# Performance work log

Measured on AMD Instinct MI355X. Metric: run time of the kernel, lower is better.

## Reference

```python
import jax, jax.numpy as jnp
import numpy as np

B, S, H, E, TOPK = 16384, 64, 256, 8, 2


def setup_inputs() -> dict:
    key = jax.random.key(0)
    k1, k2, k3, k4 = jax.random.split(key, 4)
    x = jax.random.normal(k1, (B, S, H), dtype=jnp.float32)
    xr = jax.random.normal(k2, (B, H), dtype=jnp.float32)
    W_router = jax.random.normal(k3, (H, E), dtype=jnp.float32) * 0.02
    W_experts = jax.random.normal(k4, (E, H, H), dtype=jnp.float32) * 0.02
    b_experts = jnp.zeros((E, H), dtype=jnp.float32)
    return {"x": x, "xr": xr, "W_router": W_router,
            "W_experts": W_experts, "b_experts": b_experts}


def reference(x, xr, W_router, W_experts, b_experts):
    # Routing network: logits [B, E]
    logits = xr @ W_router
    # top-2 expert selection; softmax over the two selected logits (as in torch code)
    top_vals, top_idx = jax.lax.top_k(logits, TOPK)          # [B, 2]
    w = jax.nn.softmax(top_vals, axis=1)                     # [B, 2]
    # Dense gate matrix [B, E]: scatter top-2 weights into expert slots
    gate = jnp.zeros_like(logits).at[jnp.arange(x.shape[0])[:, None], top_idx].add(w)
    # Expert forward: pooled token representation -> per-expert dense tanh
    pooled = x.mean(axis=1)                                  # [B, H]
    h_all = jnp.tanh(jnp.einsum('bh,ehd->bed', pooled, W_experts) + b_experts[None])
    # Weighted scatter-add combine: prediction[b] += w * hidden_states
    prediction = jnp.einsum('be,beh->bh', gate, h_all)       # [B, H]
    return prediction
```

## Files before the change

kernel.cpp:

```cpp
#include <hip/hip_runtime.h>
#include <hip/hip_bf16.h>

constexpr int Bn = 16384;
constexpr int S  = 64;
constexpr int H  = 256;
constexpr int E  = 8;

constexpr int RPB  = 32;
constexpr int CBLK = Bn / RPB;
constexpr int TPB  = 512;
constexpr int PSTR = H + 8;

typedef short bf16x8 __attribute__((ext_vector_type(8)));
typedef float f32x4  __attribute__((ext_vector_type(4)));

__device__ __forceinline__ float fast_tanh(float x) {
    const float ex = __expf(2.0f * x);
    return (ex - 1.0f) / (ex + 1.0f);
}

__global__ __launch_bounds__(256) void prep_wfrag(const float* __restrict__ We,
                                                  __hip_bfloat16* __restrict__ Wf) {
    __shared__ __hip_bfloat16 tile[64][H + 4];
    const int e    = blockIdx.x >> 2;
    const int hblk = blockIdx.x & 3;
    const int t    = threadIdx.x;

    const float* src = We + ((size_t)e * H + hblk * 64) * H;
#pragma unroll
    for (int i = 0; i < 16; ++i) {
        const int idx = t + 256 * i;
        const int hh  = idx >> 6;
        const int c4  = idx & 63;
        float4 v = reinterpret_cast<const float4*>(src + (size_t)hh * H)[c4];
        tile[hh][c4 * 4 + 0] = __float2bfloat16(v.x);
        tile[hh][c4 * 4 + 1] = __float2bfloat16(v.y);
        tile[hh][c4 * 4 + 2] = __float2bfloat16(v.z);
        tile[hh][c4 * 4 + 3] = __float2bfloat16(v.w);
    }
    __syncthreads();

#pragma unroll
    for (int i = 0; i < 8; ++i) {
        const int task = i * 256 + t;
        const int kk2  = task >> 10;
        const int nt   = (task >> 6) & 15;
        const int l    = task & 63;
        const int kk   = hblk * 2 + kk2;
        const int hlb  = kk2 * 32 + (l >> 4) * 8;
        const int d    = nt * 16 + (l & 15);
        bf16x8 p;
#pragma unroll
        for (int j = 0; j < 8; ++j) {
            __hip_bfloat16 hv = tile[hlb + j][d];
            p[j] = *reinterpret_cast<short*>(&hv);
        }
        reinterpret_cast<bf16x8*>(Wf)[(((size_t)(e * 8 + kk) * 16 + nt) * 64 + l)] = p;
    }
}

__global__ __launch_bounds__(256) void pool_kernel(const float* __restrict__ x,
                                                   __hip_bfloat16* __restrict__ pws) {
    const int t   = threadIdx.x;
    const int row = blockIdx.x * 4 + (t >> 6);
    const int c4  = t & 63;

    const float4* xrow = reinterpret_cast<const float4*>(x + (size_t)row * (S * H));
    float4 a0 = make_float4(0.f,0.f,0.f,0.f), a1 = a0, a2 = a0, a3 = a0;
#pragma unroll 16
    for (int s = 0; s < S; s += 4) {
        float4 v0 = xrow[(s + 0) * 64 + c4];
        float4 v1 = xrow[(s + 1) * 64 + c4];
        float4 v2 = xrow[(s + 2) * 64 + c4];
        float4 v3 = xrow[(s + 3) * 64 + c4];
        a0.x += v0.x; a0.y += v0.y; a0.z += v0.z; a0.w += v0.w;
        a1.x += v1.x; a1.y += v1.y; a1.z += v1.z; a1.w += v1.w;
        a2.x += v2.x; a2.y += v2.y; a2.z += v2.z; a2.w += v2.w;
        a3.x += v3.x; a3.y += v3.y; a3.z += v3.z; a3.w += v3.w;
    }
    const float sc = 1.0f / (float)S;
    float r0 = (a0.x + a1.x) + (a2.x + a3.x);
    float r1 = (a0.y + a1.y) + (a2.y + a3.y);
    float r2 = (a0.z + a1.z) + (a2.z + a3.z);
    float r3 = (a0.w + a1.w) + (a2.w + a3.w);
    ushort4 pk;
    {
        __hip_bfloat16 h0 = __float2bfloat16(r0 * sc);
        __hip_bfloat16 h1 = __float2bfloat16(r1 * sc);
        __hip_bfloat16 h2 = __float2bfloat16(r2 * sc);
        __hip_bfloat16 h3 = __float2bfloat16(r3 * sc);
        pk.x = *reinterpret_cast<unsigned short*>(&h0);
        pk.y = *reinterpret_cast<unsigned short*>(&h1);
        pk.z = *reinterpret_cast<unsigned short*>(&h2);
        pk.w = *reinterpret_cast<unsigned short*>(&h3);
    }
    *reinterpret_cast<ushort4*>(pws + (size_t)row * H + c4 * 4) = pk;
}

__global__ __launch_bounds__(TPB, 4) void combine_kernel(
    const __hip_bfloat16* __restrict__ pws,
    const float* __restrict__ xr,
    const float* __restrict__ Wr,
    const float* __restrict__ be,
    const __hip_bfloat16* __restrict__ Wf,
    float* __restrict__ out)
{
    const int b0 = blockIdx.x * RPB;
    const int t  = threadIdx.x;

    __shared__ __hip_bfloat16 pooled[RPB][PSTR];
    __shared__ float logit_s[RPB][E];
    __shared__ float gate_s[RPB][E];

    {
        const __hip_bfloat16* src = pws + (size_t)b0 * H + t * 16;
#pragma unroll
        for (int u = 0; u < 2; ++u) {
            const int g = t * 16 + u * 8;
            bf16x8 v = *reinterpret_cast<const bf16x8*>(src + u * 8);
            *reinterpret_cast<bf16x8*>(&pooled[g >> 8][g & 255]) = v;
        }
    }

    if (t < RPB * E) {
        const int r = t >> 3, e = t & 7;
        const float* xrp = xr + (size_t)(b0 + r) * H;
        double acc = 0.0;
#pragma unroll 8
        for (int h = 0; h < H; ++h)
            acc += (double)xrp[h] * (double)Wr[h * E + e];
        logit_s[r][e] = (float)acc;
    }
    __syncthreads();

    if (t < RPB) {
        int i0 = 0; float v0 = logit_s[t][0];
#pragma unroll
        for (int e = 1; e < E; ++e)
            if (logit_s[t][e] > v0) { v0 = logit_s[t][e]; i0 = e; }
        int i1 = -1; float v1 = -3.0e38f;
#pragma unroll
        for (int e = 0; e < E; ++e) {
            if (e == i0) continue;
            if (logit_s[t][e] > v1) { v1 = logit_s[t][e]; i1 = e; }
        }
        const float ex  = expf(v1 - v0);
        const float inv = 1.0f / (1.0f + ex);
#pragma unroll
        for (int e = 0; e < E; ++e) gate_s[t][e] = 0.f;
        gate_s[t][i0] = inv;
        gate_s[t][i1] = ex * inv;
    }
    __syncthreads();

    {
        const int w  = t >> 6;
        const int l  = t & 63;
        const int rg = w >> 2;
        const int dg = w & 3;
        const int lr = l & 15;
        const int lq = l >> 4;

        f32x4 oacc[4];
#pragma unroll
        for (int n = 0; n < 4; ++n) oacc[n] = 0.f;

        const __hip_bfloat16* abase = &pooled[rg * 16 + lr][lq * 8];
        const bf16x8* wf8 = reinterpret_cast<const bf16x8*>(Wf);

        for (int e = 0; e < E; ++e) {
            f32x4 acc[4];
#pragma unroll
            for (int n = 0; n < 4; ++n) acc[n] = 0.f;

#pragma unroll
            for (int kk = 0; kk < 8; ++kk) {
                const bf16x8 a = *reinterpret_cast<const bf16x8*>(abase + kk * 32);
                const size_t kb = ((size_t)(e * 8 + kk) * 16 + dg * 4) * 64 + l;
                bf16x8 bfr[4];
#pragma unroll
                for (int n = 0; n < 4; ++n)
                    bfr[n] = wf8[kb + (size_t)n * 64];
#pragma unroll
                for (int n = 0; n < 4; ++n)
                    acc[n] = __builtin_amdgcn_mfma_f32_16x16x32_bf16(a, bfr[n], acc[n], 0, 0, 0);
            }

            float g[4];
#pragma unroll
            for (int j = 0; j < 4; ++j) g[j] = gate_s[rg * 16 + lq * 4 + j][e];
#pragma unroll
            for (int n = 0; n < 4; ++n) {
                const int d = dg * 64 + n * 16 + lr;
                const float bias = be[e * H + d];
#pragma unroll
                for (int j = 0; j < 4; ++j)
                    oacc[n][j] += g[j] * fast_tanh(acc[n][j] + bias);
            }
        }

#pragma unroll
        for (int n = 0; n < 4; ++n) {
            const int d = dg * 64 + n * 16 + lr;
#pragma unroll
            for (int j = 0; j < 4; ++j) {
                const int r = rg * 16 + lq * 4 + j;
                out[(size_t)(b0 + r) * H + d] = oacc[n][j];
            }
        }
    }
}

__global__ __launch_bounds__(256) void moe_fused_fallback(
    const float* __restrict__ x, const float* __restrict__ xr,
    const float* __restrict__ Wr, const float* __restrict__ We,
    const float* __restrict__ be, float* __restrict__ out)
{
    const int b = blockIdx.x;
    const int t = threadIdx.x;

    __shared__ float  pooled[H];
    __shared__ float  xr_s[H];
    __shared__ float4 red4[4][64];
    __shared__ float  logits_s[E];
    __shared__ int    sel[2];
    __shared__ float  wsel[2];

    {
        const float4* xrow = reinterpret_cast<const float4*>(x + (size_t)b * S * H);
        const int c4 = t & 63;
        const int sg = t >> 6;
        float4 acc = make_float4(0.f, 0.f, 0.f, 0.f);
#pragma unroll
        for (int i = 0; i < 16; ++i) {
            float4 v = xrow[(sg + 4 * i) * 64 + c4];
            acc.x += v.x; acc.y += v.y; acc.z += v.z; acc.w += v.w;
        }
        red4[sg][c4] = acc;
        xr_s[t] = xr[(size_t)b * H + t];
    }
    __syncthreads();
    {
        const float* r0 = reinterpret_cast<const float*>(&red4[0][0]);
        const float* r1 = reinterpret_cast<const float*>(&red4[1][0]);
        const float* r2 = reinterpret_cast<const float*>(&red4[2][0]);
        const float* r3 = reinterpret_cast<const float*>(&red4[3][0]);
        pooled[t] = (r0[t] + r1[t] + r2[t] + r3[t]) * (1.0f / (float)S);
    }
    if (t < E) {
        double acc = 0.0;
        for (int h = 0; h < H; ++h)
            acc += (double)xr_s[h] * (double)Wr[h * E + t];
        logits_s[t] = (float)acc;
    }
    __syncthreads();
    if (t == 0) {
        int i0 = 0; float v0 = logits_s[0];
        for (int e = 1; e < E; ++e)
            if (logits_s[e] > v0) { v0 = logits_s[e]; i0 = e; }
        int i1 = -1; float v1 = -3.0e38f;
        for (int e = 0; e < E; ++e) {
            if (e == i0) continue;
            if (logits_s[e] > v1) { v1 = logits_s[e]; i1 = e; }
        }
        const float ex = expf(v1 - v0);
        const float inv = 1.0f / (1.0f + ex);
        sel[0] = i0; sel[1] = i1;
        wsel[0] = inv; wsel[1] = ex * inv;
    }
    __syncthreads();
    {
        const int   e0 = sel[0], e1 = sel[1];
        const float w0 = wsel[0], w1 = wsel[1];
        const float* W0 = We + (size_t)e0 * H * H + t;
        const float* W1 = We + (size_t)e1 * H * H + t;
        float a0 = be[e0 * H + t];
        float a1 = be[e1 * H + t];
#pragma unroll 8
        for (int h = 0; h < H; ++h) {
            const float p = pooled[h];
            a0 = fmaf(p, W0[(size_t)h * H], a0);
            a1 = fmaf(p, W1[(size_t)h * H], a1);
        }
        out[(size_t)b * H + t] = w0 * tanhf(a0) + w1 * tanhf(a1);
    }
}

extern "C" void kernel_launch(void* const* d_in, const int* in_sizes, int n_in,
                              void* d_out, int out_size, void* d_ws, size_t ws_size,
                              hipStream_t stream) {
    const float* x  = (const float*)d_in[0];
    const float* xr = (const float*)d_in[1];
    const float* Wr = (const float*)d_in[2];
    const float* We = (const float*)d_in[3];
    const float* be = (const float*)d_in[4];
    float* out = (float*)d_out;

    (void)in_sizes; (void)n_in; (void)out_size;

    const size_t wf_elems = (size_t)E * H * H;
    const size_t need = (wf_elems + (size_t)Bn * H) * sizeof(__hip_bfloat16);
    if (ws_size >= need) {
        __hip_bfloat16* Wf  = (__hip_bfloat16*)d_ws;
        __hip_bfloat16* pws = Wf + wf_elems;
        prep_wfrag<<<32, 256, 0, stream>>>(We, Wf);
        pool_kernel<<<Bn / 4, 256, 0, stream>>>(x, pws);
        combine_kernel<<<CBLK, TPB, 0, stream>>>(pws, xr, Wr, be, Wf, out);
    } else {
        moe_fused_fallback<<<Bn, 256, 0, stream>>>(x, xr, Wr, We, be, out);
    }
}
```

Before: 275.7 us.

## Merge pool and weight-prep kernels; restructure combine to 4 waves with 2 row tiles

```diff
diff --git a/kernel.cpp b/kernel.cpp
--- a/kernel.cpp
+++ b/kernel.cpp
@@ -8,8 +8,10 @@
 
 constexpr int RPB  = 32;
 constexpr int CBLK = Bn / RPB;
-constexpr int TPB  = 512;
 constexpr int PSTR = H + 8;
+
+constexpr int POOLB = Bn / 4;
+constexpr int PREPB = E * 8;
 
 typedef short bf16x8 __attribute__((ext_vector_type(8)));
 typedef float f32x4  __attribute__((ext_vector_type(4)));
@@ -19,85 +21,81 @@
     return (ex - 1.0f) / (ex + 1.0f);
 }
 
-__global__ __launch_bounds__(256) void prep_wfrag(const float* __restrict__ We,
-                                                  __hip_bfloat16* __restrict__ Wf) {
-    __shared__ __hip_bfloat16 tile[64][H + 4];
-    const int e    = blockIdx.x >> 2;
-    const int hblk = blockIdx.x & 3;
-    const int t    = threadIdx.x;
-
-    const float* src = We + ((size_t)e * H + hblk * 64) * H;
-#pragma unroll
-    for (int i = 0; i < 16; ++i) {
-        const int idx = t + 256 * i;
-        const int hh  = idx >> 6;
-        const int c4  = idx & 63;
-        float4 v = reinterpret_cast<const float4*>(src + (size_t)hh * H)[c4];
-        tile[hh][c4 * 4 + 0] = __float2bfloat16(v.x);
-        tile[hh][c4 * 4 + 1] = __float2bfloat16(v.y);
-        tile[hh][c4 * 4 + 2] = __float2bfloat16(v.z);
-        tile[hh][c4 * 4 + 3] = __float2bfloat16(v.w);
-    }
-    __syncthreads();
-
-#pragma unroll
-    for (int i = 0; i < 8; ++i) {
-        const int task = i * 256 + t;
-        const int kk2  = task >> 10;
-        const int nt   = (task >> 6) & 15;
-        const int l    = task & 63;
-        const int kk   = hblk * 2 + kk2;
-        const int hlb  = kk2 * 32 + (l >> 4) * 8;
-        const int d    = nt * 16 + (l & 15);
-        bf16x8 p;
-#pragma unroll
-        for (int j = 0; j < 8; ++j) {
-            __hip_bfloat16 hv = tile[hlb + j][d];
-            p[j] = *reinterpret_cast<short*>(&hv);
-        }
-        reinterpret_cast<bf16x8*>(Wf)[(((size_t)(e * 8 + kk) * 16 + nt) * 64 + l)] = p;
-    }
-}
-
-__global__ __launch_bounds__(256) void pool_kernel(const float* __restrict__ x,
-                                                   __hip_bfloat16* __restrict__ pws) {
-    const int t   = threadIdx.x;
-    const int row = blockIdx.x * 4 + (t >> 6);
-    const int c4  = t & 63;
-
-    const float4* xrow = reinterpret_cast<const float4*>(x + (size_t)row * (S * H));
-    float4 a0 = make_float4(0.f,0.f,0.f,0.f), a1 = a0, a2 = a0, a3 = a0;
+__global__ __launch_bounds__(256) void stage1_kernel(
+    const float* __restrict__ x,
+    const float* __restrict__ We,
+    __hip_bfloat16* __restrict__ pws,
+    __hip_bfloat16* __restrict__ Wf)
+{
+    __shared__ __hip_bfloat16 tile[32][H + 4];
+    const int t = threadIdx.x;
+
+    if (blockIdx.x < POOLB) {
+        const int row = blockIdx.x * 4 + (t >> 6);
+        const int c4  = t & 63;
+
+        const f32x4* xrow = reinterpret_cast<const f32x4*>(x + (size_t)row * (S * H));
+        f32x4 a0 = 0.f, a1 = 0.f, a2 = 0.f, a3 = 0.f;
 #pragma unroll 16
-    for (int s = 0; s < S; s += 4) {
-        float4 v0 = xrow[(s + 0) * 64 + c4];
-        float4 v1 = xrow[(s + 1) * 64 + c4];
-        float4 v2 = xrow[(s + 2) * 64 + c4];
-        float4 v3 = xrow[(s + 3) * 64 + c4];
-        a0.x += v0.x; a0.y += v0.y; a0.z += v0.z; a0.w += v0.w;
-        a1.x += v1.x; a1.y += v1.y; a1.z += v1.z; a1.w += v1.w;
-        a2.x += v2.x; a2.y += v2.y; a2.z += v2.z; a2.w += v2.w;
-        a3.x += v3.x; a3.y += v3.y; a3.z += v3.z; a3.w += v3.w;
-    }
-    const float sc = 1.0f / (float)S;
-    float r0 = (a0.x + a1.x) + (a2.x + a3.x);
-    float r1 = (a0.y + a1.y) + (a2.y + a3.y);
-    float r2 = (a0.z + a1.z) + (a2.z + a3.z);
-    float r3 = (a0.w + a1.w) + (a2.w + a3.w);
-    ushort4 pk;
-    {
-        __hip_bfloat16 h0 = __float2bfloat16(r0 * sc);
-        __hip_bfloat16 h1 = __float2bfloat16(r1 * sc);
-        __hip_bfloat16 h2 = __float2bfloat16(r2 * sc);
-        __hip_bfloat16 h3 = __float2bfloat16(r3 * sc);
-        pk.x = *reinterpret_cast<unsigned short*>(&h0);
-        pk.y = *reinterpret_cast<unsigned short*>(&h1);
-        pk.z = *reinterpret_cast<unsigned short*>(&h2);
-        pk.w = *reinterpret_cast<unsigned short*>(&h3);
-    }
-    *reinterpret_cast<ushort4*>(pws + (size_t)row * H + c4 * 4) = pk;
-}
-
-__global__ __launch_bounds__(TPB, 4) void combine_kernel(
+        for (int s = 0; s < S; s += 4) {
+            f32x4 v0 = __builtin_nontemporal_load(xrow + (s + 0) * 64 + c4);
+            f32x4 v1 = __builtin_nontemporal_load(xrow + (s + 1) * 64 + c4);
+            f32x4 v2 = __builtin_nontemporal_load(xrow + (s + 2) * 64 + c4);
+            f32x4 v3 = __builtin_nontemporal_load(xrow + (s + 3) * 64 + c4);
+            a0 += v0; a1 += v1; a2 += v2; a3 += v3;
+        }
+        const f32x4 res = (a0 + a1) + (a2 + a3);
+        const float sc = 1.0f / (float)S;
+        ushort4 pk;
+        {
+            __hip_bfloat16 h0 = __float2bfloat16(res[0] * sc);
+            __hip_bfloat16 h1 = __float2bfloat16(res[1] * sc);
+            __hip_bfloat16 h2 = __float2bfloat16(res[2] * sc);
+            __hip_bfloat16 h3 = __float2bfloat16(res[3] * sc);
+            pk.x = *reinterpret_cast<unsigned short*>(&h0);
+            pk.y = *reinterpret_cast<unsigned short*>(&h1);
+            pk.z = *reinterpret_cast<unsigned short*>(&h2);
+            pk.w = *reinterpret_cast<unsigned short*>(&h3);
+        }
+        *reinterpret_cast<ushort4*>(pws + (size_t)row * H + c4 * 4) = pk;
+    } else {
+        const int bid = blockIdx.x - POOLB;
+        const int e   = bid >> 3;
+        const int kk  = bid & 7;
+
+        const float* src = We + ((size_t)e * H + kk * 32) * H;
+#pragma unroll
+        for (int i = 0; i < 8; ++i) {
+            const int idx = t + 256 * i;
+            const int hh  = idx >> 6;
+            const int c4  = idx & 63;
+            float4 v = reinterpret_cast<const float4*>(src + (size_t)hh * H)[c4];
+            tile[hh][c4 * 4 + 0] = __float2bfloat16(v.x);
+            tile[hh][c4 * 4 + 1] = __float2bfloat16(v.y);
+            tile[hh][c4 * 4 + 2] = __float2bfloat16(v.z);
+            tile[hh][c4 * 4 + 3] = __float2bfloat16(v.w);
+        }
+        __syncthreads();
+
+#pragma unroll
+        for (int i = 0; i < 4; ++i) {
+            const int task = i * 256 + t;
+            const int nt_  = task >> 6;
+            const int l    = task & 63;
+            const int hlb  = (l >> 4) * 8;
+            const int d    = nt_ * 16 + (l & 15);
+            bf16x8 p;
+#pragma unroll
+            for (int j = 0; j < 8; ++j) {
+                __hip_bfloat16 hv = tile[hlb + j][d];
+                p[j] = *reinterpret_cast<short*>(&hv);
+            }
+            reinterpret_cast<bf16x8*>(Wf)[(((size_t)(e * 8 + kk) * 16 + nt_) * 64 + l)] = p;
+        }
+    }
+}
+
+__global__ __launch_bounds__(256, 2) void combine_kernel(
     const __hip_bfloat16* __restrict__ pws,
     const float* __restrict__ xr,
     const float* __restrict__ Wr,
@@ -113,16 +111,16 @@
     __shared__ float gate_s[RPB][E];
 
     {
-        const __hip_bfloat16* src = pws + (size_t)b0 * H + t * 16;
-#pragma unroll
-        for (int u = 0; u < 2; ++u) {
-            const int g = t * 16 + u * 8;
+        const __hip_bfloat16* src = pws + (size_t)b0 * H + t * 32;
+#pragma unroll
+        for (int u = 0; u < 4; ++u) {
+            const int g = t * 32 + u * 8;
             bf16x8 v = *reinterpret_cast<const bf16x8*>(src + u * 8);
             *reinterpret_cast<bf16x8*>(&pooled[g >> 8][g & 255]) = v;
         }
     }
 
-    if (t < RPB * E) {
+    {
         const int r = t >> 3, e = t & 7;
         const float* xrp = xr + (size_t)(b0 + r) * H;
         double acc = 0.0;
@@ -154,60 +152,73 @@
     __syncthreads();
 
     {
-        const int w  = t >> 6;
+        const int dg = t >> 6;
         const int l  = t & 63;
-        const int rg = w >> 2;
-        const int dg = w & 3;
         const int lr = l & 15;
         const int lq = l >> 4;
 
-        f32x4 oacc[4];
-#pragma unroll
-        for (int n = 0; n < 4; ++n) oacc[n] = 0.f;
-
-        const __hip_bfloat16* abase = &pooled[rg * 16 + lr][lq * 8];
+        f32x4 oacc[2][4];
+#pragma unroll
+        for (int m = 0; m < 2; ++m)
+#pragma unroll
+            for (int n = 0; n < 4; ++n) oacc[m][n] = 0.f;
+
+        const __hip_bfloat16* a0base = &pooled[lr][lq * 8];
+        const __hip_bfloat16* a1base = &pooled[16 + lr][lq * 8];
         const bf16x8* wf8 = reinterpret_cast<const bf16x8*>(Wf);
 
         for (int e = 0; e < E; ++e) {
-            f32x4 acc[4];
-#pragma unroll
-            for (int n = 0; n < 4; ++n) acc[n] = 0.f;
+            f32x4 acc[2][4];
+#pragma unroll
+            for (int m = 0; m < 2; ++m)
+#pragma unroll
+                for (int n = 0; n < 4; ++n) acc[m][n] = 0.f;
 
 #pragma unroll
             for (int kk = 0; kk < 8; ++kk) {
-                const bf16x8 a = *reinterpret_cast<const bf16x8*>(abase + kk * 32);
+                const bf16x8 a0 = *reinterpret_cast<const bf16x8*>(a0base + kk * 32);
+                const bf16x8 a1 = *reinterpret_cast<const bf16x8*>(a1base + kk * 32);
                 const size_t kb = ((size_t)(e * 8 + kk) * 16 + dg * 4) * 64 + l;
                 bf16x8 bfr[4];
 #pragma unroll
                 for (int n = 0; n < 4; ++n)
                     bfr[n] = wf8[kb + (size_t)n * 64];
 #pragma unroll
-                for (int n = 0; n < 4; ++n)
-                    acc[n] = __builtin_amdgcn_mfma_f32_16x16x32_bf16(a, bfr[n], acc[n], 0, 0, 0);
+                for (int n = 0; n < 4; ++n) {
+                    acc[0][n] = __builtin_amdgcn_mfma_f32_16x16x32_bf16(a0, bfr[n], acc[0][n], 0, 0, 0);
+                    acc[1][n] = __builtin_amdgcn_mfma_f32_16x16x32_bf16(a1, bfr[n], acc[1][n], 0, 0, 0);
+                }
             }
 
-            float g[4];
-#pragma unroll
-            for (int j = 0; j < 4; ++j) g[j] = gate_s[rg * 16 + lq * 4 + j][e];
+            float g[2][4];
+#pragma unroll
+            for (int m = 0; m < 2; ++m)
+#pragma unroll
+                for (int j = 0; j < 4; ++j)
+                    g[m][j] = gate_s[m * 16 + lq * 4 + j][e];
 #pragma unroll
             for (int n = 0; n < 4; ++n) {
                 const int d = dg * 64 + n * 16 + lr;
                 const float bias = be[e * H + d];
 #pragma unroll
-                for (int j = 0; j < 4; ++j)
-                    oacc[n][j] += g[j] * fast_tanh(acc[n][j] + bias);
+                for (int m = 0; m < 2; ++m)
+#pragma unroll
+                    for (int j = 0; j < 4; ++j)
+                        oacc[m][n][j] += g[m][j] * fast_tanh(acc[m][n][j] + bias);
             }
         }
 
 #pragma unroll
-        for (int n = 0; n < 4; ++n) {
-            const int d = dg * 64 + n * 16 + lr;
-#pragma unroll
-            for (int j = 0; j < 4; ++j) {
-                const int r = rg * 16 + lq * 4 + j;
-                out[(size_t)(b0 + r) * H + d] = oacc[n][j];
+        for (int m = 0; m < 2; ++m)
+#pragma unroll
+            for (int n = 0; n < 4; ++n) {
+                const int d = dg * 64 + n * 16 + lr;
+#pragma unroll
+                for (int j = 0; j < 4; ++j) {
+                    const int r = m * 16 + lq * 4 + j;
+                    out[(size_t)(b0 + r) * H + d] = oacc[m][n][j];
+                }
             }
-        }
     }
 }
 
@@ -303,9 +314,8 @@
     if (ws_size >= need) {
         __hip_bfloat16* Wf  = (__hip_bfloat16*)d_ws;
         __hip_bfloat16* pws = Wf + wf_elems;
-        prep_wfrag<<<32, 256, 0, stream>>>(We, Wf);
-        pool_kernel<<<Bn / 4, 256, 0, stream>>>(x, pws);
-        combine_kernel<<<CBLK, TPB, 0, stream>>>(pws, xr, Wr, be, Wf, out);
+        stage1_kernel<<<POOLB + PREPB, 256, 0, stream>>>(x, We, pws, Wf);
+        combine_kernel<<<CBLK, 256, 0, stream>>>(pws, xr, Wr, be, Wf, out);
     } else {
         moe_fused_fallback<<<Bn, 256, 0, stream>>>(x, xr, Wr, We, be, out);
     }
```

Result: faster. 241.4 us (-12.4%).
